# Kernel tuning notes

Measured on AMD Instinct MI355X. Metric: run time of the kernel, lower is better.

Reference implementation:

```python
import jax, jax.numpy as jnp
import numpy as np

B, L, D, H = 4, 2048, 512, 8
HD = D // H  # 64
MAX_REL = 4


def setup_inputs() -> dict:
    key = jax.random.key(0)
    ks = jax.random.split(key, 13)
    s = 1.0 / np.sqrt(D)
    return {
        "q": jax.random.normal(ks[0], (B, L, D), jnp.float32),
        "k": jax.random.normal(ks[1], (B, L, D), jnp.float32),
        "v": jax.random.normal(ks[2], (B, L, D), jnp.float32),
        "Wq": jax.random.normal(ks[3], (D, D), jnp.float32) * s,
        "bq": jax.random.normal(ks[4], (D,), jnp.float32) * 0.01,
        "Wk": jax.random.normal(ks[5], (D, D), jnp.float32) * s,
        "bk": jax.random.normal(ks[6], (D,), jnp.float32) * 0.01,
        "Wv": jax.random.normal(ks[7], (D, D), jnp.float32) * s,
        "bv": jax.random.normal(ks[8], (D,), jnp.float32) * 0.01,
        "Wo": jax.random.normal(ks[9], (D, D), jnp.float32) * s,
        "bo": jax.random.normal(ks[10], (D,), jnp.float32) * 0.01,
        "rel_k_table": jax.random.normal(ks[11], (2 * MAX_REL + 1, HD), jnp.float32),
        "rel_v_table": jax.random.normal(ks[12], (2 * MAX_REL + 1, HD), jnp.float32),
    }


def _to_heads(x):
    # [B, L, D] -> [B, H, L, HD]
    b, l, d = x.shape
    return x.reshape(b, l, H, d // H).transpose(0, 2, 1, 3)


def reference(q, k, v, Wq, bq, Wk, bk, Wv, bv, Wo, bo, rel_k_table, rel_v_table):
    # NOTE: in the source, the relative-attention output is overwritten by the
    # plain SDPA call immediately after, so observable math = SDPA only.
    # rel_k_table / rel_v_table are dead parameters (zero gradient).
    relu = jax.nn.relu
    qh = _to_heads(relu(q @ Wq.T + bq))  # [B,H,L,HD]
    kh = _to_heads(relu(k @ Wk.T + bk))
    vh = _to_heads(relu(v @ Wv.T + bv))
    # scale by sqrt(d_key)=sqrt(512), matching the original (not sqrt(head_dim))
    scores = jnp.einsum("bhqd,bhkd->bhqk", qh, kh) / jnp.sqrt(jnp.float32(D))
    attn = jax.nn.softmax(scores, axis=-1)
    out = jnp.einsum("bhqk,bhkd->bhqd", attn, vh)  # [B,H,L,HD]
    out = out.transpose(0, 2, 1, 3).reshape(B, L, D)
    return relu(out @ Wo.T + bo)
```

## Files before the change

### kernel.cpp

```cpp
#include <hip/hip_runtime.h>
#include <hip/hip_bf16.h>

#define B_  4
#define L_  2048
#define D_  512
#define H_  8
#define HD_ 64
#define M_  (B_ * L_)

typedef __bf16 bf16;
typedef __attribute__((ext_vector_type(8)))  __bf16 bf16x8;
typedef __attribute__((ext_vector_type(4)))  __bf16 bf16x4;
typedef __attribute__((ext_vector_type(16))) float  f32x16;

__device__ __forceinline__ f32x16 mfma32(bf16x8 a, bf16x8 b, f32x16 c) {
    return __builtin_amdgcn_mfma_f32_32x32x16_bf16(a, b, c, 0, 0, 0);
}

__device__ __forceinline__ void pack_body(const float* __restrict__ src,
                                          bf16* __restrict__ dst, int R,
                                          int m0, int k0)
{
    __shared__ __align__(16) bf16 tile[64][76];
    const int t = threadIdx.x;
#pragma unroll
    for (int rep = 0; rep < 4; rep++) {
        const int idx = rep * 256 + t;
        const int r = idx >> 4, c4 = idx & 15;
        const float4 f = *(const float4*)(src + (size_t)(m0 + r) * 512 + k0 + c4 * 4);
        bf16x4 v; v[0] = (bf16)f.x; v[1] = (bf16)f.y; v[2] = (bf16)f.z; v[3] = (bf16)f.w;
        *(bf16x4*)(&tile[r][c4 * 4]) = v;
    }
    __syncthreads();
#pragma unroll
    for (int rep = 0; rep < 2; rep++) {
        const int s = rep * 256 + t;
        const int ml = s & 63, kpl = s >> 6;
        const bf16x4 lo = *(const bf16x4*)(&tile[ml][kpl * 8]);
        const bf16x4 hi4 = *(const bf16x4*)(&tile[ml][kpl * 8 + 4]);
        bf16x8 v;
#pragma unroll
        for (int e = 0; e < 4; e++) { v[e] = lo[e]; v[e + 4] = hi4[e]; }
        *(bf16x8*)(dst + ((size_t)(k0 / 8 + kpl) * R + m0 + ml) * 8) = v;
    }
}

__global__ __launch_bounds__(256) void pack_w(
    const float* __restrict__ W0, const float* __restrict__ W1,
    const float* __restrict__ W2, const float* __restrict__ W3,
    bf16* __restrict__ Wp)
{
    const int z = blockIdx.z;
    const float* src = z == 0 ? W0 : z == 1 ? W1 : z == 2 ? W2 : W3;
    pack_body(src, Wp + (size_t)z * 64 * 512 * 8, 512, blockIdx.x * 64, blockIdx.y * 64);
}

struct PJob {
    const bf16* X; const float* Xf; const bf16* W; const float* bias;
    void* out; float postmul; int mode;
};

__device__ __forceinline__ void barrier_lds_only()
{
    asm volatile("s_waitcnt lgkmcnt(0)" ::: "memory");
    __builtin_amdgcn_s_barrier();
}

template<bool FP32A>
__device__ __forceinline__ void proj_body(const PJob jb)
{
    const int w    = threadIdx.x >> 6;
    const int lane = threadIdx.x & 63;
    const int l31  = lane & 31;
    const int hi   = lane >> 5;
    const int m0 = blockIdx.x * 128;
    const int n0 = blockIdx.y * 128;
    const int mh = w & 1;
    const int nh = w >> 1;

    __shared__ __align__(16) bf16 Ab[2][8][64][8];
    __shared__ __align__(16) bf16 Bb[2][8][64][8];

    f32x16 acc[2][2];
#pragma unroll
    for (int mi = 0; mi < 2; mi++)
#pragma unroll
        for (int ni = 0; ni < 2; ni++)
#pragma unroll
            for (int r = 0; r < 16; r++) acc[mi][ni][r] = 0.0f;

    auto ldA = [&](int f, int k0) -> bf16x8 {
        return *(const bf16x8*)(jb.X + ((size_t)((k0 >> 3) + (f >> 2) * 2 + hi) * M_
                                        + m0 + (f & 3) * 32 + l31) * 8);
    };
    auto ldB = [&](int f, int k0) -> bf16x8 {
        return *(const bf16x8*)(jb.W + ((size_t)((k0 >> 3) + (f >> 2) * 2 + hi) * 512
                                        + n0 + (f & 3) * 32 + l31) * 8);
    };

    bf16x8 rA[2][2], rB[2][2];
    float4 rT[2][4];

    auto ldT = [&](int s, int k0) {
#pragma unroll
        for (int rep = 0; rep < 4; rep++) {
            const int idx = rep * 256 + (int)threadIdx.x;
            rT[s][rep] = *(const float4*)(jb.Xf + (size_t)(m0 + (idx >> 3)) * 512
                                          + k0 + (idx & 7) * 4);
        }
    };
    auto stA = [&](int s, int buf) {
#pragma unroll
        for (int rep = 0; rep < 4; rep++) {
            const int idx = rep * 256 + (int)threadIdx.x;
            const int r = idx >> 3, c4 = idx & 7;
            const float4 f = rT[s][rep];
            bf16x4 v; v[0] = (bf16)f.x; v[1] = (bf16)f.y;
            v[2] = (bf16)f.z; v[3] = (bf16)f.w;
            const int fs = ((c4 >> 2) << 2) | (r >> 5);
            const int ln = (r & 31) | (((c4 >> 1) & 1) << 5);
            *(bf16x4*)(&Ab[buf][fs][ln][(c4 & 1) * 4]) = v;
        }
    };

    if constexpr (FP32A) {
        ldT(0, 0); stA(0, 0); ldT(1, 32); ldT(0, 64);
    } else {
#pragma unroll
        for (int i = 0; i < 2; i++) rA[0][i] = ldA(w * 2 + i, 0);
#pragma unroll
        for (int i = 0; i < 2; i++)
            *(bf16x8*)(&Ab[0][w * 2 + i][lane][0]) = rA[0][i];
#pragma unroll
        for (int i = 0; i < 2; i++) rA[1][i] = ldA(w * 2 + i, 32);
#pragma unroll
        for (int i = 0; i < 2; i++) rA[0][i] = ldA(w * 2 + i, 64);
    }
#pragma unroll
    for (int i = 0; i < 2; i++) rB[0][i] = ldB(w * 2 + i, 0);
#pragma unroll
    for (int i = 0; i < 2; i++)
        *(bf16x8*)(&Bb[0][w * 2 + i][lane][0]) = rB[0][i];
#pragma unroll
    for (int i = 0; i < 2; i++) rB[1][i] = ldB(w * 2 + i, 32);
#pragma unroll
    for (int i = 0; i < 2; i++) rB[0][i] = ldB(w * 2 + i, 64);
    __syncthreads();

#pragma unroll
    for (int it = 0; it < 16; it++) {
        const int cur = it & 1;
#pragma unroll
        for (int ks = 0; ks < 2; ks++) {
            const bf16x8 a0 = *(const bf16x8*)(&Ab[cur][ks * 4 + mh * 2 + 0][lane][0]);
            const bf16x8 a1 = *(const bf16x8*)(&Ab[cur][ks * 4 + mh * 2 + 1][lane][0]);
            const bf16x8 b0 = *(const bf16x8*)(&Bb[cur][ks * 4 + nh * 2 + 0][lane][0]);
            const bf16x8 b1 = *(const bf16x8*)(&Bb[cur][ks * 4 + nh * 2 + 1][lane][0]);
            acc[0][0] = mfma32(a0, b0, acc[0][0]);
            acc[0][1] = mfma32(a0, b1, acc[0][1]);
            acc[1][0] = mfma32(a1, b0, acc[1][0]);
            acc[1][1] = mfma32(a1, b1, acc[1][1]);
        }
        if (it < 15) {
            const int s = (it + 1) & 1;
            if constexpr (FP32A) {
                stA(s, 1 - cur);
            } else {
#pragma unroll
                for (int i = 0; i < 2; i++)
                    *(bf16x8*)(&Ab[1 - cur][w * 2 + i][lane][0]) = rA[s][i];
            }
#pragma unroll
            for (int i = 0; i < 2; i++)
                *(bf16x8*)(&Bb[1 - cur][w * 2 + i][lane][0]) = rB[s][i];
            if (it < 13) {
                if constexpr (FP32A) {
                    ldT(s, (it + 3) * 32);
                } else {
#pragma unroll
                    for (int i = 0; i < 2; i++)
                        rA[s][i] = ldA(w * 2 + i, (it + 3) * 32);
                }
#pragma unroll
                for (int i = 0; i < 2; i++)
                    rB[s][i] = ldB(w * 2 + i, (it + 3) * 32);
            }
            barrier_lds_only();
        }
    }

    const int mode = jb.mode;
#pragma unroll
    for (int ni = 0; ni < 2; ni++) {
        const int col = n0 + (nh * 2 + ni) * 32 + l31;
        const float bn = jb.bias[col];
#pragma unroll
        for (int mi = 0; mi < 2; mi++)
#pragma unroll
            for (int r = 0; r < 16; r++) {
                const int row = m0 + (mh * 2 + mi) * 32 + (r & 3) + 8 * (r >> 2) + 4 * hi;
                float v = fmaxf(acc[mi][ni][r] + bn, 0.0f);
                if (mode == 2) {
                    ((float*)jb.out)[(size_t)row * D_ + col] = v;
                } else {
                    v *= jb.postmul;
                    const int b = row >> 11, l = row & (L_ - 1);
                    const int h = col >> 6,  hd = col & (HD_ - 1);
                    const int bh = b * H_ + h;
                    size_t idx;
                    if (mode == 0) {
                        idx = ((size_t)bh * L_ + l) * HD_ + hd;
                    } else if (mode == 1) {
                        idx = (((size_t)bh * 8 + (hd >> 3)) * L_ + l) * 8 + (hd & 7);
                    } else {
                        const int swzl = (l & ~15) | (l & 3) | ((l & 4) << 1) | ((l & 8) >> 1);
                        idx = (((size_t)bh * 256 + (swzl >> 3)) * 64 + hd) * 8 + (swzl & 7);
                    }
                    ((bf16*)jb.out)[idx] = (bf16)v;
                }
            }
    }
}

__global__ __launch_bounds__(256, 3) void proj_kernel(PJob j0, PJob j1, PJob j2)
{
    const PJob jb = (blockIdx.z == 0) ? j0 : (blockIdx.z == 1) ? j1 : j2;
    proj_body<false>(jb);
}

__global__ __launch_bounds__(256, 3) void proj_qkv_kernel(PJob j0, PJob j1, PJob j2)
{
    const PJob jb = (blockIdx.z == 0) ? j0 : (blockIdx.z == 1) ? j1 : j2;
    proj_body<true>(jb);
}

__global__ __launch_bounds__(128, 2) void attn_kernel(
    const bf16* __restrict__ qh, const bf16* __restrict__ Kp,
    const bf16* __restrict__ Vp, bf16* __restrict__ Op)
{
    const int w    = threadIdx.x >> 6;
    const int lane = threadIdx.x & 63;
    const int l31  = lane & 31;
    const int hi   = lane >> 5;

    const int lin  = blockIdx.x + (blockIdx.y << 5);
    const int xcd  = lin & 7;
    const int slot = lin >> 3;
    const int bh   = (xcd << 2) + (slot >> 5);
    const int qb   = (slot & 31) * 64 + w * 32;

    const bf16* Q   = qh + (size_t)bh * L_ * HD_;
    const bf16* Kpb = Kp + (size_t)bh * 8 * L_ * 8;
    const bf16* Vpb = Vp + (size_t)bh * 256 * 64 * 8;

    __shared__ __align__(16) bf16 Vb[2][8][64][8];

    bf16x8 qf[4];
#pragma unroll
    for (int ks = 0; ks < 4; ks++)
        qf[ks] = *(const bf16x8*)(Q + (size_t)(qb + l31) * HD_ + ks * 16 + hi * 8);

    f32x16 zz;
#pragma unroll
    for (int r = 0; r < 16; r++) zz[r] = 0.0f;
    f32x16 o0 = zz, o1 = zz, lacc = zz;
    bf16x8 ones;
#pragma unroll
    for (int u = 0; u < 8; u++) ones[u] = (bf16)1.0f;

    auto ldK = [&](int f, int t) -> bf16x8 {
        return *(const bf16x8*)(Kpb + ((size_t)((f >> 1) * 2 + hi) * L_
                                       + t * 64 + (f & 1) * 32 + l31) * 8);
    };
    auto ldV = [&](int f, int t) -> bf16x8 {
        return *(const bf16x8*)(Vpb + ((size_t)(t * 8 + (f >> 1) * 2 + hi) * 64
                                       + (f & 1) * 32 + l31) * 8);
    };

    bf16x8 kr[8], vr[2][4];
#pragma unroll
    for (int i = 0; i < 4; i++) vr[0][i] = ldV(w * 4 + i, 0);
#pragma unroll
    for (int i = 0; i < 4; i++) *(bf16x8*)(&Vb[0][w * 4 + i][lane][0]) = vr[0][i];
#pragma unroll
    for (int i = 0; i < 4; i++) vr[1][i] = ldV(w * 4 + i, 1);
#pragma unroll
    for (int i = 0; i < 4; i++) vr[0][i] = ldV(w * 4 + i, 2);
#pragma unroll
    for (int f = 0; f < 8; f++) kr[f] = ldK(f, 0);
    __syncthreads();

    auto tile_body = [&](int t, int cur, int nxt) {
        f32x16 s0 = mfma32(kr[0], qf[0], zz);
        f32x16 s1 = mfma32(kr[1], qf[0], zz);
#pragma unroll
        for (int ks = 1; ks < 4; ks++) {
            s0 = mfma32(kr[ks * 2 + 0], qf[ks], s0);
            s1 = mfma32(kr[ks * 2 + 1], qf[ks], s1);
        }
        if (t < 31) {
#pragma unroll
            for (int f = 0; f < 8; f++) kr[f] = ldK(f, t + 1);
        }

#pragma unroll
        for (int r = 0; r < 16; r++) s0[r] = __builtin_amdgcn_exp2f(s0[r]);
        {
            bf16x8 pf0, pf1;
#pragma unroll
            for (int u = 0; u < 8; u++) { pf0[u] = (bf16)s0[u]; pf1[u] = (bf16)s0[8 + u]; }
            o0   = mfma32(pf0, *(const bf16x8*)(&Vb[cur][0][lane][0]), o0);
            o1   = mfma32(pf0, *(const bf16x8*)(&Vb[cur][1][lane][0]), o1);
            lacc = mfma32(pf0, ones, lacc);
            o0   = mfma32(pf1, *(const bf16x8*)(&Vb[cur][2][lane][0]), o0);
            o1   = mfma32(pf1, *(const bf16x8*)(&Vb[cur][3][lane][0]), o1);
            lacc = mfma32(pf1, ones, lacc);
        }
#pragma unroll
        for (int r = 0; r < 16; r++) s1[r] = __builtin_amdgcn_exp2f(s1[r]);
        {
            bf16x8 pf2, pf3;
#pragma unroll
            for (int u = 0; u < 8; u++) { pf2[u] = (bf16)s1[u]; pf3[u] = (bf16)s1[8 + u]; }
            o0   = mfma32(pf2, *(const bf16x8*)(&Vb[cur][4][lane][0]), o0);
            o1   = mfma32(pf2, *(const bf16x8*)(&Vb[cur][5][lane][0]), o1);
            lacc = mfma32(pf2, ones, lacc);
            o0   = mfma32(pf3, *(const bf16x8*)(&Vb[cur][6][lane][0]), o0);
            o1   = mfma32(pf3, *(const bf16x8*)(&Vb[cur][7][lane][0]), o1);
            lacc = mfma32(pf3, ones, lacc);
        }

        if (t < 31) {
#pragma unroll
            for (int i = 0; i < 4; i++)
                *(bf16x8*)(&Vb[1 - cur][w * 4 + i][lane][0]) = vr[nxt][i];
            const int tn = (t + 3 < 32) ? t + 3 : 31;
#pragma unroll
            for (int i = 0; i < 4; i++) vr[nxt][i] = ldV(w * 4 + i, tn);
            __syncthreads();
        }
    };

    for (int tt = 0; tt < 16; tt++) {
        tile_body(2 * tt + 0, 0, 1);
        tile_body(2 * tt + 1, 1, 0);
    }

    const int b = bh >> 3, h = bh & 7;
#pragma unroll
    for (int r = 0; r < 16; r++) {
        const int rl = (r & 3) + 8 * (r >> 2) + 4 * hi;
        const float inv = 1.0f / lacc[r];
        const int m = b * L_ + qb + rl;
        const int c0 = h * HD_ + l31;
        Op[((size_t)(c0 >> 3) * M_ + m) * 8 + (c0 & 7)] = (bf16)(o0[r] * inv);
        const int c1 = c0 + 32;
        Op[((size_t)(c1 >> 3) * M_ + m) * 8 + (c1 & 7)] = (bf16)(o1[r] * inv);
    }
}

extern "C" void kernel_launch(void* const* d_in, const int* in_sizes, int n_in,
                              void* d_out, int out_size, void* d_ws, size_t ws_size,
                              hipStream_t stream)
{
    (void)in_sizes; (void)n_in; (void)out_size; (void)ws_size;
    const float* q  = (const float*)d_in[0];
    const float* k  = (const float*)d_in[1];
    const float* v  = (const float*)d_in[2];
    const float* Wq = (const float*)d_in[3];
    const float* bq = (const float*)d_in[4];
    const float* Wk = (const float*)d_in[5];
    const float* bk = (const float*)d_in[6];
    const float* Wv = (const float*)d_in[7];
    const float* bv = (const float*)d_in[8];
    const float* Wo = (const float*)d_in[9];
    const float* bo = (const float*)d_in[10];
    float* out = (float*)d_out;

    char* ws = (char*)d_ws;
    const size_t MB = 1024 * 1024;
    bf16* Vp  = (bf16*)(ws);
    bf16* Opb = (bf16*)(ws + 8 * MB);
    bf16* Wp  = (bf16*)(ws + 16 * MB);
    bf16* qh  = (bf16*)(d_out);
    bf16* Kp  = (bf16*)((char*)d_out + 8 * MB);

    bf16* Wqp = Wp;
    bf16* Wkp = Wp + (size_t)64 * 512 * 8;
    bf16* Wvp = Wp + (size_t)2 * 64 * 512 * 8;
    bf16* Wop = Wp + (size_t)3 * 64 * 512 * 8;

    const float SCALE_LOG2E = 0.06377946282349575f;

    pack_w<<<dim3(8, 8, 4), dim3(256), 0, stream>>>(Wq, Wk, Wv, Wo, Wp);

    PJob jq{nullptr, q, Wqp, bq, qh, SCALE_LOG2E, 0};
    PJob jk{nullptr, k, Wkp, bk, Kp, 1.0f, 1};
    PJob jv{nullptr, v, Wvp, bv, Vp, 1.0f, 3};
    proj_qkv_kernel<<<dim3(64, 4, 3), dim3(256), 0, stream>>>(jq, jk, jv);

    attn_kernel<<<dim3(32, 32), dim3(128), 0, stream>>>(qh, Kp, Vp, Opb);

    PJob jo{Opb, nullptr, Wop, bo, out, 1.0f, 2};
    proj_kernel<<<dim3(64, 4, 1), dim3(256), 0, stream>>>(jo, jo, jo);
}
```

Baseline: 194.1 us.

## Specialize output projection kernel with narrower N tile, deeper K step and 3-stage prefetch

Replaces the templated bf16-input projection path with a dedicated output-projection kernel. It uses 128x64 tiles, which doubles the grid to 512 blocks for better CU occupancy. It uses a K step of 64 with a three-deep register prefetch ring, halving the number of barriers per tile. The trade is less operand reuse per block (each A tile is loaded twice across N) and more registers for the prefetch buffers.

```diff
diff --git a/kernel.cpp b/kernel.cpp
--- a/kernel.cpp
+++ b/kernel.cpp
@@ -66,9 +66,33 @@
     __builtin_amdgcn_s_barrier();
 }
 
-template<bool FP32A>
-__device__ __forceinline__ void proj_body(const PJob jb)
-{
+__device__ __forceinline__ void proj_epilogue_elem(const PJob& jb, int row,
+                                                   int col, float v)
+{
+    const int mode = jb.mode;
+    if (mode == 2) {
+        ((float*)jb.out)[(size_t)row * D_ + col] = v;
+    } else {
+        v *= jb.postmul;
+        const int b = row >> 11, l = row & (L_ - 1);
+        const int h = col >> 6,  hd = col & (HD_ - 1);
+        const int bh = b * H_ + h;
+        size_t idx;
+        if (mode == 0) {
+            idx = ((size_t)bh * L_ + l) * HD_ + hd;
+        } else if (mode == 1) {
+            idx = (((size_t)bh * 8 + (hd >> 3)) * L_ + l) * 8 + (hd & 7);
+        } else {
+            const int swzl = (l & ~15) | (l & 3) | ((l & 4) << 1) | ((l & 8) >> 1);
+            idx = (((size_t)bh * 256 + (swzl >> 3)) * 64 + hd) * 8 + (swzl & 7);
+        }
+        ((bf16*)jb.out)[idx] = (bf16)v;
+    }
+}
+
+__global__ __launch_bounds__(256, 3) void proj_qkv_kernel(PJob j0, PJob j1, PJob j2)
+{
+    const PJob jb = (blockIdx.z == 0) ? j0 : (blockIdx.z == 1) ? j1 : j2;
     const int w    = threadIdx.x >> 6;
     const int lane = threadIdx.x & 63;
     const int l31  = lane & 31;
@@ -89,16 +113,12 @@
 #pragma unroll
             for (int r = 0; r < 16; r++) acc[mi][ni][r] = 0.0f;
 
-    auto ldA = [&](int f, int k0) -> bf16x8 {
-        return *(const bf16x8*)(jb.X + ((size_t)((k0 >> 3) + (f >> 2) * 2 + hi) * M_
-                                        + m0 + (f & 3) * 32 + l31) * 8);
-    };
     auto ldB = [&](int f, int k0) -> bf16x8 {
         return *(const bf16x8*)(jb.W + ((size_t)((k0 >> 3) + (f >> 2) * 2 + hi) * 512
                                         + n0 + (f & 3) * 32 + l31) * 8);
     };
 
-    bf16x8 rA[2][2], rB[2][2];
+    bf16x8 rB[2][2];
     float4 rT[2][4];
 
     auto ldT = [&](int s, int k0) {
@@ -123,19 +143,7 @@
         }
     };
 
-    if constexpr (FP32A) {
-        ldT(0, 0); stA(0, 0); ldT(1, 32); ldT(0, 64);
-    } else {
-#pragma unroll
-        for (int i = 0; i < 2; i++) rA[0][i] = ldA(w * 2 + i, 0);
-#pragma unroll
-        for (int i = 0; i < 2; i++)
-            *(bf16x8*)(&Ab[0][w * 2 + i][lane][0]) = rA[0][i];
-#pragma unroll
-        for (int i = 0; i < 2; i++) rA[1][i] = ldA(w * 2 + i, 32);
-#pragma unroll
-        for (int i = 0; i < 2; i++) rA[0][i] = ldA(w * 2 + i, 64);
-    }
+    ldT(0, 0); stA(0, 0); ldT(1, 32); ldT(0, 64);
 #pragma unroll
     for (int i = 0; i < 2; i++) rB[0][i] = ldB(w * 2 + i, 0);
 #pragma unroll
@@ -163,24 +171,12 @@
         }
         if (it < 15) {
             const int s = (it + 1) & 1;
-            if constexpr (FP32A) {
-                stA(s, 1 - cur);
-            } else {
-#pragma unroll
-                for (int i = 0; i < 2; i++)
-                    *(bf16x8*)(&Ab[1 - cur][w * 2 + i][lane][0]) = rA[s][i];
-            }
+            stA(s, 1 - cur);
 #pragma unroll
             for (int i = 0; i < 2; i++)
                 *(bf16x8*)(&Bb[1 - cur][w * 2 + i][lane][0]) = rB[s][i];
             if (it < 13) {
-                if constexpr (FP32A) {
-                    ldT(s, (it + 3) * 32);
-                } else {
-#pragma unroll
-                    for (int i = 0; i < 2; i++)
-                        rA[s][i] = ldA(w * 2 + i, (it + 3) * 32);
-                }
+                ldT(s, (it + 3) * 32);
 #pragma unroll
                 for (int i = 0; i < 2; i++)
                     rB[s][i] = ldB(w * 2 + i, (it + 3) * 32);
@@ -189,7 +185,6 @@
         }
     }
 
-    const int mode = jb.mode;
 #pragma unroll
     for (int ni = 0; ni < 2; ni++) {
         const int col = n0 + (nh * 2 + ni) * 32 + l31;
@@ -199,39 +194,96 @@
 #pragma unroll
             for (int r = 0; r < 16; r++) {
                 const int row = m0 + (mh * 2 + mi) * 32 + (r & 3) + 8 * (r >> 2) + 4 * hi;
-                float v = fmaxf(acc[mi][ni][r] + bn, 0.0f);
-                if (mode == 2) {
-                    ((float*)jb.out)[(size_t)row * D_ + col] = v;
-                } else {
-                    v *= jb.postmul;
-                    const int b = row >> 11, l = row & (L_ - 1);
-                    const int h = col >> 6,  hd = col & (HD_ - 1);
-                    const int bh = b * H_ + h;
-                    size_t idx;
-                    if (mode == 0) {
-                        idx = ((size_t)bh * L_ + l) * HD_ + hd;
-                    } else if (mode == 1) {
-                        idx = (((size_t)bh * 8 + (hd >> 3)) * L_ + l) * 8 + (hd & 7);
-                    } else {
-                        const int swzl = (l & ~15) | (l & 3) | ((l & 4) << 1) | ((l & 8) >> 1);
-                        idx = (((size_t)bh * 256 + (swzl >> 3)) * 64 + hd) * 8 + (swzl & 7);
-                    }
-                    ((bf16*)jb.out)[idx] = (bf16)v;
-                }
+                proj_epilogue_elem(jb, row, col, fmaxf(acc[mi][ni][r] + bn, 0.0f));
             }
     }
 }
 
-__global__ __launch_bounds__(256, 3) void proj_kernel(PJob j0, PJob j1, PJob j2)
-{
-    const PJob jb = (blockIdx.z == 0) ? j0 : (blockIdx.z == 1) ? j1 : j2;
-    proj_body<false>(jb);
-}
-
-__global__ __launch_bounds__(256, 3) void proj_qkv_kernel(PJob j0, PJob j1, PJob j2)
-{
-    const PJob jb = (blockIdx.z == 0) ? j0 : (blockIdx.z == 1) ? j1 : j2;
-    proj_body<true>(jb);
+__global__ __launch_bounds__(256, 3) void proj_o_kernel(PJob jb)
+{
+    const int w    = threadIdx.x >> 6;
+    const int lane = threadIdx.x & 63;
+    const int l31  = lane & 31;
+    const int hi   = lane >> 5;
+    const int m0 = blockIdx.x * 128;
+    const int n0 = blockIdx.y * 64;
+    const int mh = w & 1;
+    const int nh = w >> 1;
+
+    __shared__ __align__(16) bf16 Ab[2][16][64][8];
+    __shared__ __align__(16) bf16 Bb[2][8][64][8];
+
+    f32x16 acc[2];
+#pragma unroll
+    for (int mi = 0; mi < 2; mi++)
+#pragma unroll
+        for (int r = 0; r < 16; r++) acc[mi][r] = 0.0f;
+
+    auto ldA = [&](int f, int k0) -> bf16x8 {
+        return *(const bf16x8*)(jb.X + ((size_t)((k0 >> 3) + (f >> 2) * 2 + hi) * M_
+                                        + m0 + (f & 3) * 32 + l31) * 8);
+    };
+    auto ldB = [&](int f, int k0) -> bf16x8 {
+        return *(const bf16x8*)(jb.W + ((size_t)((k0 >> 3) + (f >> 1) * 2 + hi) * 512
+                                        + n0 + (f & 1) * 32 + l31) * 8);
+    };
+
+    bf16x8 rA[3][4], rB[3][2];
+#pragma unroll
+    for (int i = 0; i < 4; i++) rA[0][i] = ldA(w * 4 + i, 0);
+#pragma unroll
+    for (int i = 0; i < 2; i++) rB[0][i] = ldB(w * 2 + i, 0);
+#pragma unroll
+    for (int i = 0; i < 4; i++) *(bf16x8*)(&Ab[0][w * 4 + i][lane][0]) = rA[0][i];
+#pragma unroll
+    for (int i = 0; i < 2; i++) *(bf16x8*)(&Bb[0][w * 2 + i][lane][0]) = rB[0][i];
+#pragma unroll
+    for (int s = 1; s < 3; s++) {
+#pragma unroll
+        for (int i = 0; i < 4; i++) rA[s][i] = ldA(w * 4 + i, s * 64);
+#pragma unroll
+        for (int i = 0; i < 2; i++) rB[s][i] = ldB(w * 2 + i, s * 64);
+    }
+    __syncthreads();
+
+#pragma unroll
+    for (int it = 0; it < 8; it++) {
+        const int cur = it & 1;
+        if (it < 5) {
+            const int s = it % 3, kn = (it + 3) * 64;
+#pragma unroll
+            for (int i = 0; i < 4; i++) rA[s][i] = ldA(w * 4 + i, kn);
+#pragma unroll
+            for (int i = 0; i < 2; i++) rB[s][i] = ldB(w * 2 + i, kn);
+        }
+#pragma unroll
+        for (int ks = 0; ks < 4; ks++) {
+            const bf16x8 bfr = *(const bf16x8*)(&Bb[cur][ks * 2 + nh][lane][0]);
+#pragma unroll
+            for (int mi = 0; mi < 2; mi++) {
+                const bf16x8 afr = *(const bf16x8*)(&Ab[cur][ks * 4 + mh * 2 + mi][lane][0]);
+                acc[mi] = mfma32(afr, bfr, acc[mi]);
+            }
+        }
+        if (it < 7) {
+            const int s = (it + 1) % 3;
+#pragma unroll
+            for (int i = 0; i < 4; i++) *(bf16x8*)(&Ab[1 - cur][w * 4 + i][lane][0]) = rA[s][i];
+#pragma unroll
+            for (int i = 0; i < 2; i++) *(bf16x8*)(&Bb[1 - cur][w * 2 + i][lane][0]) = rB[s][i];
+            __syncthreads();
+        }
+    }
+
+    const int col = n0 + nh * 32 + l31;
+    const float bn = jb.bias[col];
+#pragma unroll
+    for (int mi = 0; mi < 2; mi++)
+#pragma unroll
+        for (int r = 0; r < 16; r++) {
+            const int row = m0 + (mh * 2 + mi) * 32 + (r & 3) + 8 * (r >> 2) + 4 * hi;
+            proj_epilogue_elem(jb, row, col, fmaxf(acc[mi][r] + bn, 0.0f));
+        }
 }
 
 __global__ __launch_bounds__(128, 2) void attn_kernel(
@@ -402,5 +454,5 @@
     attn_kernel<<<dim3(32, 32), dim3(128), 0, stream>>>(qh, Kp, Vp, Opb);
 
     PJob jo{Opb, nullptr, Wop, bo, out, 1.0f, 2};
-    proj_kernel<<<dim3(64, 4, 1), dim3(256), 0, stream>>>(jo, jo, jo);
-}
+    proj_o_kernel<<<dim3(64, 8), dim3(256), 0, stream>>>(jo);
+}
```

New measurement: 191.5 us, median of 3. Within noise of the previous version (-1.3%).
